# Kernel tuning notes

Measured on AMD Instinct MI355X. Metric: run time of the kernel, lower is better.

Reference implementation:

```python
import jax, jax.numpy as jnp
import numpy as np

PRE = 2000          # pre_wbf_detections
POST = 300          # post_wbf_detections
IOU_THRESH = 0.55   # wbf_iou_thresh
NUM_CLASSES = 5


def setup_inputs() -> dict:
    key = jax.random.key(0)
    k1, k2, k3, k4 = jax.random.split(key, 4)
    # realistic xyxy boxes in a 1024px image
    ctr = jax.random.uniform(k1, (PRE, 2), minval=0.0, maxval=1024.0)
    wh = jax.random.uniform(k2, (PRE, 2), minval=8.0, maxval=96.0)
    boxes = jnp.concatenate([ctr - wh / 2, ctr + wh / 2], axis=1)
    scores = jax.random.uniform(k3, (PRE, 1), minval=0.05, maxval=1.0)
    labels = jax.random.randint(k4, (PRE, 1), 0, NUM_CLASSES).astype(jnp.float32)
    x = jnp.concatenate([boxes, scores, labels], axis=1)  # (PRE, 6)
    return {"x": x}


def _iou_one_vs_many(box, mboxes):
    # torchvision-style box_iou of one box (4,) vs many (N,4)
    lt = jnp.maximum(box[:2], mboxes[:, :2])
    rb = jnp.minimum(box[2:], mboxes[:, 2:])
    wh = jnp.clip(rb - lt, 0.0)
    inter = wh[:, 0] * wh[:, 1]
    a1 = (box[2] - box[0]) * (box[3] - box[1])
    a2 = (mboxes[:, 2] - mboxes[:, 0]) * (mboxes[:, 3] - mboxes[:, 1])
    union = a1 + a2 - inter
    safe = jnp.where(union > 0, union, 1.0)
    return jnp.where(union > 0, inter / safe, 0.0)


def _wbf_forward(x):
    # Sequential WBF clustering. The torch code runs wbf() per unique class;
    # since a detection can only join a cluster of its own class and cluster
    # creation order within a class is preserved, a single sequential pass
    # with a class-equality check is mathematically identical (final result
    # is sorted by score, so per-class concatenation order is irrelevant).
    N = x.shape[0]
    # cluster state: score-weighted box sum, score sum, member count, class, valid
    init = (
        jnp.zeros((N, 4), x.dtype),   # sum of score*box per cluster
        jnp.zeros((N,), x.dtype),     # sum of scores per cluster
        jnp.zeros((N,), jnp.int32),   # member count per cluster
        jnp.zeros((N,), x.dtype),     # class id per cluster
        jnp.zeros((N,), bool),        # cluster slot valid
    )

    def step(carry, det):
        sum_wb, sum_s, cnt, cls, valid = carry
        box, score, c = det[:4], det[4], det[5]
        denom = jnp.where(valid, sum_s, 1.0)
        mboxes = sum_wb / denom[:, None]  # current merged boxes
        iou = _iou_one_vs_many(box, mboxes)
        match = valid & (cls == c) & (iou > IOU_THRESH)
        found = jnp.any(match)
        first = jnp.argmax(match)                  # first matching cluster
        n_valid = jnp.sum(valid).astype(jnp.int32)  # next free slot
        idx = jnp.where(found, first, n_valid)
        sum_wb = sum_wb.at[idx].add(score * box)
        sum_s = sum_s.at[idx].add(score)
        cnt = cnt.at[idx].add(1)
        cls = cls.at[idx].set(c)
        valid = valid.at[idx].set(True)
        return (sum_wb, sum_s, cnt, cls, valid), None

    (sum_wb, sum_s, cnt, cls, valid), _ = jax.lax.scan(step, init, x)

    denom = jnp.where(valid, sum_s, 1.0)
    boxes = sum_wb / denom[:, None]                              # weighted avg box
    scores = sum_s / jnp.maximum(cnt.astype(x.dtype), 1.0)       # mean score
    sort_key = jnp.where(valid, scores, -1.0)
    order = jnp.argsort(-sort_key)                               # descending by score
    top = order[:POST]
    vtop = valid[top]
    out = jnp.concatenate(
        [boxes[top], scores[top, None], cls[top, None]], axis=1)  # (POST, 6)
    return jnp.where(vtop[:, None], out, 0.0)


def reference(x):
    return _wbf_forward(x[:PRE])
```

## Files before the change

### kernel.cpp

```cpp
#include <hip/hip_runtime.h>

typedef unsigned long long u64;
typedef unsigned short u16;
typedef unsigned u32;
typedef unsigned char u8;

#define PRE   2000
#define POST  300
#define NCLS  5
#define CAP   512
#define INF   0x7fffffff
#define MAGIC 0x13579BDFu
#define NBLK  21
#define SORTB 20

#define MID 0x1.19999A8p-1

template <int K> struct IC { static constexpr int v = K; };
template <int N, typename F> __device__ __forceinline__ void unrollN(F&& f) {
    if constexpr (N > 0) { unrollN<N - 1>(f); f(IC<N - 1>{}); }
}

__device__ __forceinline__ u32 aload_acq(u32* p) {
    return __hip_atomic_load(p, __ATOMIC_ACQUIRE, __HIP_MEMORY_SCOPE_AGENT);
}

__device__ __forceinline__ float rlF(float v, int l) {
    return __uint_as_float((u32)__builtin_amdgcn_readlane((int)__float_as_uint(v), l));
}

__device__ __forceinline__ bool iou_pred(float bx0, float bx1, float bx2, float bx3,
                                         float a1, float m0, float m1, float m2, float m3,
                                         float a2) {
    const float ltx = fmaxf(bx0, m0), lty = fmaxf(bx1, m1);
    const float rbx = fminf(bx2, m2), rby = fminf(bx3, m3);
    const float wd = fmaxf(rbx - ltx, 0.f), hg = fmaxf(rby - lty, 0.f);
    const float inter = wd * hg;
    const float uni = (a1 + a2) - inter;
    return (uni > 0.f) && ((double)inter >= MID * (double)uni);
}

__global__ __launch_bounds__(512, 1) void wbf_all(const float* __restrict__ x,
                                                  u64* __restrict__ M,
                                                  u32* __restrict__ ctrl,
                                                  float* __restrict__ recs,
                                                  int* __restrict__ cnts,
                                                  float* __restrict__ out) {
#pragma clang fp contract(off)
    __shared__ __align__(16) char s_buf[58448];
    u8*  s_mtx = (u8*)s_buf;
    float (*s_det)[8]  = (float (*)[8])(s_buf + 32768);
    float (*s_dov)[16] = (float (*)[16])(s_buf + 49152);
    u16* s_list        = (u16*)(s_buf + 57344);
    u8*  s_ab          = (u8*)(s_buf + 58376);

    const int tid  = threadIdx.x;
    const int lane = tid & 63;
    const int wave = tid >> 6;
    const int b    = blockIdx.x;

    if (b == 0) {
        if (tid == 0) {
            for (int i = 0; i < NCLS; ++i)
                __hip_atomic_store(&ctrl[i], 0u, __ATOMIC_RELAXED, __HIP_MEMORY_SCOPE_AGENT);
            __hip_atomic_store(&ctrl[16], 0u, __ATOMIC_RELAXED, __HIP_MEMORY_SCOPE_AGENT);
            __hip_atomic_store(&ctrl[32], MAGIC, __ATOMIC_RELEASE, __HIP_MEMORY_SCOPE_AGENT);
        }
    } else {
        if (tid == 0) { while (aload_acq(&ctrl[32]) != MAGIC) {} }
    }
    __syncthreads();

    if (b == SORTB) {
        u64* keys = (u64*)s_buf;
        u32* hist = (u32*)(s_buf + 16384);
        u64* cand = (u64*)(s_buf + 32768);
        u32* part = (u32*)(s_buf + 36864);
        int* scal = (int*)(s_buf + 38912);

        for (int i = tid; i < 2048; i += 512) keys[i] = ~0ull;
        for (int h = tid; h < 4096; h += 512) hist[h] = 0u;
        if (tid == 0) scal[2] = 0;
        __syncthreads();
        if (tid == 0) { while (aload_acq(&ctrl[16]) < (u32)NCLS) {} }
        __syncthreads();

        int c[NCLS], off[NCLS];
        int n = 0;
        #pragma unroll
        for (int w = 0; w < NCLS; ++w) { c[w] = cnts[w]; off[w] = n; n += c[w]; }
        if (n > 2048) n = 2048;

        #pragma unroll
        for (int w = 0; w < NCLS; ++w) {
            const int cw = c[w], ow = off[w];
            for (int j = tid; j < cw; j += 512) {
                const float* r = recs + (size_t)(w * CAP + j) * 8;
                const unsigned sb = __float_as_uint(r[4]);
                const int g = ((const int*)r)[5];
                const int id = w * CAP + j;
                u64 key = ((u64)sb << 32) | ((u64)(unsigned)(0xFFFF - g) << 16) | (u64)id;
                keys[ow + j] = ~key;
            }
        }
        __syncthreads();

        for (int i = tid; i < n; i += 512)
            atomicAdd(&hist[(u32)(keys[i] >> 52)], 1u);
        __syncthreads();

        const int target = (POST < n) ? POST : n;
        u32 p = 0;
        #pragma unroll
        for (int k = 0; k < 8; ++k) p += hist[tid * 8 + k];
        part[tid] = p;
        __syncthreads();
        for (int o2 = 1; o2 < 512; o2 <<= 1) {
            const u32 v = part[tid];
            const u32 add = (tid >= o2) ? part[tid - o2] : 0u;
            __syncthreads();
            part[tid] = v + add;
            __syncthreads();
        }
        const u32 I = part[tid];
        const u32 E = I - p;
        if ((int)E < target && (int)I >= target) { scal[0] = tid; scal[1] = (int)E; }
        __syncthreads();
        const int T = scal[0];
        int cum = scal[1];
        int B = T * 8 + 7;
        for (int bb = T * 8; bb < T * 8 + 8; ++bb) {
            const int h = (int)hist[bb];
            if (cum + h >= target) { B = bb; break; }
            cum += h;
        }
        const int candCount = cum + (int)hist[B];

        if (candCount <= 512) {
            for (int i = tid; i < n; i += 512) {
                const u64 kk = keys[i];
                if ((int)(u32)(kk >> 52) <= B) {
                    const int pos = atomicAdd(&scal[2], 1);
                    cand[pos] = kk;
                }
            }
            __syncthreads();
            if (tid >= candCount) cand[tid] = ~0ull;
            __syncthreads();
            for (int kk2 = 2; kk2 <= 512; kk2 <<= 1) {
                for (int jj = kk2 >> 1; jj > 0; jj >>= 1) {
                    const int i = tid, ixj = i ^ jj;
                    if (ixj > i) {
                        const u64 a = cand[i], bb2 = cand[ixj];
                        const bool up = ((i & kk2) == 0);
                        if ((a > bb2) == up) { cand[i] = bb2; cand[ixj] = a; }
                    }
                    __syncthreads();
                }
            }
            if (tid < POST) {
                float* o = out + tid * 6;
                if (tid < target) {
                    const u64 key = ~cand[tid];
                    const int id = (int)(key & 0xFFFFull);
                    const float* rec = recs + (size_t)id * 8;
                    o[0] = rec[0]; o[1] = rec[1]; o[2] = rec[2]; o[3] = rec[3];
                    o[4] = __uint_as_float((unsigned)(key >> 32));
                    o[5] = (float)(id >> 9);
                } else {
                    o[0] = 0.f; o[1] = 0.f; o[2] = 0.f; o[3] = 0.f; o[4] = 0.f; o[5] = 0.f;
                }
            }
        } else {
            for (int kk2 = 2; kk2 <= 2048; kk2 <<= 1) {
                for (int jj = kk2 >> 1; jj > 0; jj >>= 1) {
                    for (int i = tid; i < 2048; i += 512) {
                        const int ixj = i ^ jj;
                        if (ixj > i) {
                            const u64 a = keys[i], bb2 = keys[ixj];
                            const bool up = ((i & kk2) == 0);
                            if ((a > bb2) == up) { keys[i] = bb2; keys[ixj] = a; }
                        }
                        __syncthreads();
                    }
                }
            }
            if (tid < POST) {
                float* o = out + tid * 6;
                if (tid < target) {
                    const u64 key = ~keys[tid];
                    const int id = (int)(key & 0xFFFFull);
                    const float* rec = recs + (size_t)id * 8;
                    o[0] = rec[0]; o[1] = rec[1]; o[2] = rec[2]; o[3] = rec[3];
                    o[4] = __uint_as_float((unsigned)(key >> 32));
                    o[5] = (float)(id >> 9);
                } else {
                    o[0] = 0.f; o[1] = 0.f; o[2] = 0.f; o[3] = 0.f; o[4] = 0.f; o[5] = 0.f;
                }
            }
        }
        return;
    }

    const int cls = b >> 2;
    const float mycls = (float)cls;

    int myn;
    {
        int* s_wc = (int*)s_buf;
        u64 wm[4]; int wcnt = 0;
        const int tb = wave * 256;
        #pragma unroll
        for (int i = 0; i < 4; ++i) {
            const int t = tb + i * 64 + lane;
            const bool pp = (t < PRE) && (x[t * 6 + 5] == mycls);
            wm[i] = __ballot(pp);
            wcnt += (int)__popcll(wm[i]);
        }
        if (lane == 0) s_wc[wave] = wcnt;
        __syncthreads();
        int off = 0, tot = 0;
        #pragma unroll
        for (int w = 0; w < 8; ++w) {
            const int cw = s_wc[w];
            off += (w < wave) ? cw : 0;
            tot += cw;
        }
        #pragma unroll
        for (int i = 0; i < 4; ++i) {
            const int t = tb + i * 64 + lane;
            const bool pp = ((wm[i] >> lane) & 1ull) != 0ull;
            const int pos = off + (int)__popcll(wm[i] & (((u64)1 << lane) - 1ull));
            if (pp && pos < CAP) s_list[pos] = (u16)t;
            off += (int)__popcll(wm[i]);
        }
        myn = (tot > CAP) ? CAP : tot;
        __syncthreads();
    }

    {
        float qc0[8], qc1[8], qc2[8], qc3[8], ac[8];
        unrollN<8>([&](auto k_) {
            constexpr int K = decltype(k_)::v;
            const int c = K * 64 + lane;
            qc0[K] = 0.f; qc1[K] = 0.f; qc2[K] = 0.f; qc3[K] = 0.f; ac[K] = 0.f;
            if (c < myn) {
                const int g = s_list[c];
                const float* p = x + g * 6;
                const float b0 = p[0], b1 = p[1], b2 = p[2], b3 = p[3], sc = p[4];
                qc0[K] = (sc * b0) / sc; qc1[K] = (sc * b1) / sc;
                qc2[K] = (sc * b2) / sc; qc3[K] = (sc * b3) / sc;
                ac[K] = (qc2[K] - qc0[K]) * (qc3[K] - qc1[K]);
            }
        });
        const int slice = (b & 3) * 8 + wave;
        const int rlo = slice * 16;
        const int rhi = (rlo + 16 < myn) ? rlo + 16 : myn;
        for (int r = rlo; r < rhi; ++r) {
            const int g = s_list[r];
            const float* p = x + g * 6;
            const float bx0 = p[0], bx1 = p[1], bx2 = p[2], bx3 = p[3];
            const float a1 = (bx2 - bx0) * (bx3 - bx1);
            const int Wmax = r >> 6;
            unrollN<8>([&](auto w_) {
                constexpr int W = decltype(w_)::v;
                if (W <= Wmax) {
                    const int c = W * 64 + lane;
                    const bool pred = (c < r) &&
                        iou_pred(bx0, bx1, bx2, bx3, a1, qc0[W], qc1[W], qc2[W], qc3[W], ac[W]);
                    const u64 bits = __ballot(pred);
                    if (lane == 0) M[((size_t)(cls * CAP + r)) * 8 + W] = bits;
                }
            });
        }
    }
    __threadfence();
    if (lane == 0)
        __hip_atomic_fetch_add(&ctrl[cls], 1u, __ATOMIC_RELEASE, __HIP_MEMORY_SCOPE_AGENT);

    if ((b & 3) != 0) return;

    if (lane == 0) { while (aload_acq(&ctrl[cls]) < 32u) {} }
    __syncthreads();
    {
        const ulonglong2* Mg = (const ulonglong2*)(M + (size_t)cls * CAP * 8);
        ulonglong2* Ml = (ulonglong2*)s_mtx;
        const int nit = myn * 4;
        for (int it = tid; it < nit; it += 512) Ml[it] = Mg[it];
    }
    for (int rr = tid; rr < myn; rr += 512) {
        const int g = s_list[rr];
        const float* p = x + g * 6;
        const float b0 = p[0], b1 = p[1], b2 = p[2], b3 = p[3], sc = p[4];
        s_det[rr][0] = b0; s_det[rr][1] = b1; s_det[rr][2] = b2; s_det[rr][3] = b3;
        s_det[rr][4] = sc; s_det[rr][5] = (b2 - b0) * (b3 - b1);
        ((int*)s_det[rr])[6] = g;
    }
    if (tid < 64) s_ab[tid] = 0;
    __syncthreads();
    if (wave != 0) return;

    u32 aliveB = 0;
    int dirtyCnt = 0;
    bool consA = false;
    int resCode = 0, resIdx = 0;
    float dR0 = 0.f, dR1 = 0.f, dR2 = 0.f, dR3 = 0.f, dRa = 0.f;
    float dS0 = 0.f, dS1 = 0.f, dS2 = 0.f, dS3 = 0.f, dSs = 0.f;
    int dRank = INF, dGi = 0, dCnt = 0;
    float rm0 = 0.f, rm1 = 0.f, rm2 = 0.f, rm3 = 0.f, rma = 0.f;

    auto resolve = [&](int r, float bx0, float bx1, float bx2, float bx3,
                       float sc, float a1, u32 rowByte) {
        const u32 mC = rowByte & aliveB;
        const u64 balC = __ballot(mC != 0u);
        int rank_c = INF;
        if (balC) {
            const int wl = (int)__builtin_ctzll(balC);
            const u32 byte = (u32)__builtin_amdgcn_readlane((int)mC, wl);
            rank_c = wl * 8 + (int)__builtin_ctz(byte);
        }
        const int rcs = (rank_c == INF) ? 0 : rank_c;
        const float cb0 = s_det[rcs][0], cb1 = s_det[rcs][1];
        const float cb2 = s_det[rcs][2], cb3 = s_det[rcs][3];
        const float csc = s_det[rcs][4];
        const int cgi = ((const int*)s_det[rcs])[6];

        int rank_d = INF, di = -1;
        if (dirtyCnt > 0) {
            const int DN = (dirtyCnt < 64) ? dirtyCnt : 64;
            const bool p = (lane < DN) &&
                iou_pred(bx0, bx1, bx2, bx3, a1, dR0, dR1, dR2, dR3, dRa);
            const int myrk = p ? dRank : INF;
            u64 mk = __ballot(p);
            while (mk) {
                const int l = (int)__builtin_ctzll(mk);
                mk &= mk - 1;
                const int rk = __builtin_amdgcn_readlane(myrk, l);
                if (rk < rank_d) { rank_d = rk; di = l; }
            }
            for (int dd = 64; dd < dirtyCnt; ++dd) {
                const float* dv = s_dov[dd];
                if (iou_pred(bx0, bx1, bx2, bx3, a1, dv[0], dv[1], dv[2], dv[3], dv[4])) {
                    const int rk = ((const int*)dv)[10];
                    if (rk < rank_d) { rank_d = rk; di = dd; }
                }
            }
        }
        if (rank_c == INF && rank_d == INF) {
            aliveB |= ((r >> 3) == lane) ? (1u << (r & 7)) : 0u;
            resCode = 0;
        } else if (rank_c < rank_d) {
            const int rc = rank_c;
            aliveB &= ~(((rc >> 3) == lane) ? (1u << (rc & 7)) : 0u);
            const float ns0 = (csc * cb0) + sc * bx0;
            const float ns1 = (csc * cb1) + sc * bx1;
            const float ns2 = (csc * cb2) + sc * bx2;
            const float ns3 = (csc * cb3) + sc * bx3;
            const float nss = csc + sc;
            const float nm0 = ns0 / nss, nm1 = ns1 / nss;
            const float nm2 = ns2 / nss, nm3 = ns3 / nss;
            const float nar = (nm2 - nm0) * (nm3 - nm1);
            const int D = dirtyCnt;
            if (D < 64) {
                if (lane == D) {
                    dR0 = nm0; dR1 = nm1; dR2 = nm2; dR3 = nm3; dRa = nar;
                    dS0 = ns0; dS1 = ns1; dS2 = ns2; dS3 = ns3; dSs = nss;
                    dRank = rc; dGi = cgi; dCnt = 2;
                }
            } else if (D < 128) {
                if (lane == 0) {
                    float* dv = s_dov[D];
                    dv[0] = nm0; dv[1] = nm1; dv[2] = nm2; dv[3] = nm3; dv[4] = nar;
                    dv[5] = ns0; dv[6] = ns1; dv[7] = ns2; dv[8] = ns3; dv[9] = nss;
                    ((int*)dv)[10] = rc; ((int*)dv)[11] = cgi; ((int*)dv)[12] = 2;
                }
            }
            dirtyCnt++;
            resCode = 1; resIdx = D;
            rm0 = nm0; rm1 = nm1; rm2 = nm2; rm3 = nm3; rma = nar;
        } else {
            float f0, f1, f2, f3, fs; int nct;
            if (di < 64) {
                f0 = rlF(dS0, di) + sc * bx0; f1 = rlF(dS1, di) + sc * bx1;
                f2 = rlF(dS2, di) + sc * bx2; f3 = rlF(dS3, di) + sc * bx3;
                fs = rlF(dSs, di) + sc;
                nct = __builtin_amdgcn_readlane(dCnt, di) + 1;
            } else {
                const float* dv = s_dov[di];
                f0 = dv[5] + sc * bx0; f1 = dv[6] + sc * bx1;
                f2 = dv[7] + sc * bx2; f3 = dv[8] + sc * bx3;
                fs = dv[9] + sc;
                nct = ((const int*)dv)[12] + 1;
            }
            const float nm0 = f0 / fs, nm1 = f1 / fs, nm2 = f2 / fs, nm3 = f3 / fs;
            const float nar = (nm2 - nm0) * (nm3 - nm1);
            if (di < 64) {
                if (lane == di) {
                    dR0 = nm0; dR1 = nm1; dR2 = nm2; dR3 = nm3; dRa = nar;
                    dS0 = f0; dS1 = f1; dS2 = f2; dS3 = f3; dSs = fs; dCnt = nct;
                }
            } else {
                if (lane == 0) {
                    float* dw = s_dov[di];
                    dw[0] = nm0; dw[1] = nm1; dw[2] = nm2; dw[3] = nm3; dw[4] = nar;
                    dw[5] = f0; dw[6] = f1; dw[7] = f2; dw[8] = f3; dw[9] = fs;
                    ((int*)dw)[12] = nct;
                }
            }
            rm0 = nm0; rm1 = nm1; rm2 = nm2; rm3 = nm3; rma = nar;
            resCode = 2; resIdx = di;
        }
    };

    unrollN<8>([&](auto k_) {
        constexpr int K = decltype(k_)::v;
        const int r0 = K * 64;
        if (r0 < myn) {
            const int cnt = (myn - r0 < 64) ? (myn - r0) : 64;
            const bool valid = lane < cnt;
            const u64 validM = (cnt == 64) ? ~0ull : (((u64)1 << cnt) - 1ull);
            u64 orv = 0ull;
            {
                const int rr = r0 + (valid ? lane : 0);
                const u64* rp = (const u64*)&s_mtx[(size_t)rr * 64];
                const u64* av = (const u64*)s_ab;
                unrollN<8>([&](auto w_) {
                    constexpr int W = decltype(w_)::v;
                    if (W < K)       orv |= rp[W] & av[W];
                    else if (W == K) orv |= rp[W];
                });
            }
            const u64 rowW = __ballot(valid && orv != 0ull);
            float4 db = make_float4(0.f, 0.f, 0.f, 0.f);
            float2 de = make_float2(1.f, 0.f);
            if (valid) {
                db = *(const float4*)&s_det[r0 + lane][0];
                de = *(const float2*)&s_det[r0 + lane][4];
            }
            u64 dmask = 0ull;
            if (!consA) {
                const int DN = (dirtyCnt < 64) ? dirtyCnt : 64;
                for (int d = 0; d < DN; ++d) {
                    const float m0 = rlF(dR0, d), m1 = rlF(dR1, d);
                    const float m2 = rlF(dR2, d), m3 = rlF(dR3, d);
                    const float ma = rlF(dRa, d);
                    const bool pp = valid && iou_pred(db.x, db.y, db.z, db.w, de.y,
                                                     m0, m1, m2, m3, ma);
                    if (pp) dmask |= 1ull << d;
                }
            }
            u64 danyb = __ballot(dmask != 0ull);

            u32 prB[8]; int prP[8];
            {
                u64 t = consA ? validM : ((danyb | rowW) & validM);
                #pragma unroll
                for (int i = 0; i < 8; ++i) {
                    const int f = t ? (int)__builtin_ctzll(t) : 0;
                    prP[i] = t ? f : 64;
                    prB[i] = (u32)s_mtx[(size_t)(r0 + f) * 64 + lane];
                    t &= t - 1ull;
                }
            }

            int p = 0;
            while (p < cnt) {
                u64 vm = consA ? validM : ((danyb | rowW) & validM);
                vm &= ~(((u64)1 << p) - 1ull);
                const int F = vm ? (int)__builtin_ctzll(vm) : cnt;
                {
                    const int lo = r0 + p, h2 = r0 + F;
                    int s = lo - 8 * lane; s = (s > 0) ? s : 0;
                    int e = h2 - 8 * lane; e = (e < 8) ? e : 8;
                    if (e > s) aliveB |= ((0xFFu >> (8 - (e - s))) << s);
                }
                s_ab[lane] = (u8)aliveB;
                if (F >= cnt) break;
                const int r = r0 + F;
                u32 rowByte = 0u; bool hit = false;
                #pragma unroll
                for (int i = 0; i < 8; ++i)
                    if (prP[i] == F) { rowByte = prB[i]; hit = true; }
                if (!hit) rowByte = (u32)s_mtx[(size_t)r * 64 + lane];
                const u64 balCq = __ballot((rowByte & aliveB) != 0u);
                const bool Fdirty = consA || (((danyb >> F) & 1ull) != 0ull);
                if (!Fdirty && balCq == 0ull) {
                    aliveB |= ((r >> 3) == lane) ? (1u << (r & 7)) : 0u;
                    s_ab[lane] = (u8)aliveB;
                } else {
                    const float bx0 = rlF(db.x, F), bx1 = rlF(db.y, F);
                    const float bx2 = rlF(db.z, F), bx3 = rlF(db.w, F);
                    const float sc = rlF(de.x, F), a1 = rlF(de.y, F);
                    resolve(r, bx0, bx1, bx2, bx3, sc, a1, rowByte);
                    s_ab[lane] = (u8)aliveB;
                    if (resCode != 0) {
                        const int idx = resIdx;
                        if (idx < 64) {
                            const bool pnew = valid && (lane > F) &&
                                iou_pred(db.x, db.y, db.z, db.w, de.y,
                                         rm0, rm1, rm2, rm3, rma);
                            const u64 nb = __ballot(pnew);
                            dmask = (dmask & ~(1ull << idx)) | (((nb >> lane) & 1ull) << idx);
                            danyb = __ballot(dmask != 0ull);
                        } else {
                            consA = true;
                        }
                    }
                }
                p = F + 1;
            }
        }
    });

    int wo = 0;
    for (int Kw = 0; Kw < 8; ++Kw) {
        u64 am = 0ull;
        #pragma unroll
        for (int bb = 0; bb < 8; ++bb)
            am |= (u64)(u32)(u8)__builtin_amdgcn_readlane((int)aliveB, Kw * 8 + bb) << (8 * bb);
        const int j = Kw * 64 + lane;
        const bool pred = (am >> lane) & 1ull;
        if (pred) {
            const int pos = wo + (int)__popcll(am & (((u64)1 << lane) - 1));
            const float b0 = s_det[j][0], b1 = s_det[j][1];
            const float b2 = s_det[j][2], b3 = s_det[j][3];
            const float sc = s_det[j][4];
            const int g = ((const int*)s_det[j])[6];
            float* rec = recs + (size_t)(cls * CAP + pos) * 8;
            rec[0] = (sc * b0) / sc; rec[1] = (sc * b1) / sc;
            rec[2] = (sc * b2) / sc; rec[3] = (sc * b3) / sc;
            rec[4] = sc;
            ((int*)rec)[5] = g;
        }
        wo += (int)__popcll(am);
    }
    const int demit = (dirtyCnt < 128) ? dirtyCnt : 128;
    {
        const int dreg = (demit < 64) ? demit : 64;
        if (lane < dreg) {
            float* rec = recs + (size_t)(cls * CAP + wo + lane) * 8;
            rec[0] = dR0; rec[1] = dR1; rec[2] = dR2; rec[3] = dR3;
            rec[4] = dSs / (float)dCnt;
            ((int*)rec)[5] = dGi;
        }
        for (int d = 64 + lane; d < demit; d += 64) {
            const float* dv = s_dov[d];
            float* rec = recs + (size_t)(cls * CAP + wo + d) * 8;
            rec[0] = dv[0]; rec[1] = dv[1]; rec[2] = dv[2]; rec[3] = dv[3];
            rec[4] = dv[9] / (float)(((const int*)dv)[12]);
            ((int*)rec)[5] = ((const int*)dv)[11];
        }
    }
    if (lane == 0) cnts[cls] = wo + demit;
    __threadfence();
    if (lane == 0)
        __hip_atomic_fetch_add(&ctrl[16], 1u, __ATOMIC_RELEASE, __HIP_MEMORY_SCOPE_AGENT);
}

extern "C" void kernel_launch(void* const* d_in, const int* in_sizes, int n_in,
                              void* d_out, int out_size, void* d_ws, size_t ws_size,
                              hipStream_t stream) {
    const float* x = (const float*)d_in[0];
    float* out = (float*)d_out;
    u64* M      = (u64*)d_ws;
    u32* ctrl   = (u32*)((char*)d_ws + (size_t)NCLS * CAP * 8 * 8);
    int* cnts   = (int*)((char*)d_ws + (size_t)NCLS * CAP * 8 * 8 + 256);
    float* recs = (float*)((char*)d_ws + (size_t)NCLS * CAP * 8 * 8 + 512);
    wbf_all<<<NBLK, 512, 0, stream>>>(x, M, ctrl, recs, cnts, out);
}
```

Baseline: 110.1 us.

## Stream per-class results into sorter, widen dirty mask, prefetch rows via readlane

The sort block no longer waits for all classes to finish. It polls per-class ready flags and ingests each class's records and histogram counts as soon as that class completes, so sorting work overlaps with the tail of the other classes. The IoU matrix builder loads each wave's 16 row boxes once into lanes and broadcasts them with readlane instead of doing a global load per row. The sequential resolve now tracks dirty clusters up to 128 in a two-word mask, which avoids falling back to the conservative path, and it skips the union and divide math when no lane has a positive intersection. Records are appended in completion order, so tie-breaking must still hold through the key encoding.

New measurement: 106.6 us. 3.2% less time.

```diff
diff --git a/kernel.cpp b/kernel.cpp
--- a/kernel.cpp
+++ b/kernel.cpp
@@ -63,7 +63,8 @@
         if (tid == 0) {
             for (int i = 0; i < NCLS; ++i)
                 __hip_atomic_store(&ctrl[i], 0u, __ATOMIC_RELAXED, __HIP_MEMORY_SCOPE_AGENT);
-            __hip_atomic_store(&ctrl[16], 0u, __ATOMIC_RELAXED, __HIP_MEMORY_SCOPE_AGENT);
+            for (int i = 0; i < NCLS; ++i)
+                __hip_atomic_store(&ctrl[20 + i], 0u, __ATOMIC_RELAXED, __HIP_MEMORY_SCOPE_AGENT);
             __hip_atomic_store(&ctrl[32], MAGIC, __ATOMIC_RELEASE, __HIP_MEMORY_SCOPE_AGENT);
         }
     } else {
@@ -80,34 +81,40 @@
 
         for (int i = tid; i < 2048; i += 512) keys[i] = ~0ull;
         for (int h = tid; h < 4096; h += 512) hist[h] = 0u;
-        if (tid == 0) scal[2] = 0;
+        if (tid == 0) { scal[2] = 0; scal[3] = 0; }
         __syncthreads();
-        if (tid == 0) { while (aload_acq(&ctrl[16]) < (u32)NCLS) {} }
-        __syncthreads();
-
-        int c[NCLS], off[NCLS];
-        int n = 0;
-        #pragma unroll
-        for (int w = 0; w < NCLS; ++w) { c[w] = cnts[w]; off[w] = n; n += c[w]; }
-        if (n > 2048) n = 2048;
-
-        #pragma unroll
-        for (int w = 0; w < NCLS; ++w) {
-            const int cw = c[w], ow = off[w];
-            for (int j = tid; j < cw; j += 512) {
-                const float* r = recs + (size_t)(w * CAP + j) * 8;
+
+        u32 done = 0;
+        while (done != 0x1Fu) {
+            if (tid == 0) {
+                int pick = -1;
+                while (pick < 0) {
+                    #pragma unroll
+                    for (int c = 0; c < NCLS; ++c)
+                        if (!((done >> c) & 1u) && aload_acq(&ctrl[20 + c]) == 1u) { pick = c; break; }
+                }
+                scal[4] = pick;
+                scal[5] = scal[3];
+            }
+            __syncthreads();
+            const int c = scal[4];
+            const int base = scal[5];
+            const int cw = cnts[c];
+            int take = cw; if (base + take > 2048) take = 2048 - base;
+            for (int j = tid; j < take; j += 512) {
+                const float* r = recs + (size_t)(c * CAP + j) * 8;
                 const unsigned sb = __float_as_uint(r[4]);
                 const int g = ((const int*)r)[5];
-                const int id = w * CAP + j;
+                const int id = c * CAP + j;
                 u64 key = ((u64)sb << 32) | ((u64)(unsigned)(0xFFFF - g) << 16) | (u64)id;
-                keys[ow + j] = ~key;
-            }
-        }
-        __syncthreads();
-
-        for (int i = tid; i < n; i += 512)
-            atomicAdd(&hist[(u32)(keys[i] >> 52)], 1u);
-        __syncthreads();
+                keys[base + j] = ~key;
+                atomicAdd(&hist[(u32)((~key) >> 52)], 1u);
+            }
+            if (tid == 0) scal[3] = base + take;
+            done |= 1u << c;
+            __syncthreads();
+        }
+        const int n = scal[3];
 
         const int target = (POST < n) ? POST : n;
         u32 p = 0;
@@ -256,22 +263,31 @@
         const int slice = (b & 3) * 8 + wave;
         const int rlo = slice * 16;
         const int rhi = (rlo + 16 < myn) ? rlo + 16 : myn;
-        for (int r = rlo; r < rhi; ++r) {
-            const int g = s_list[r];
-            const float* p = x + g * 6;
-            const float bx0 = p[0], bx1 = p[1], bx2 = p[2], bx3 = p[3];
-            const float a1 = (bx2 - bx0) * (bx3 - bx1);
-            const int Wmax = r >> 6;
-            unrollN<8>([&](auto w_) {
-                constexpr int W = decltype(w_)::v;
-                if (W <= Wmax) {
-                    const int c = W * 64 + lane;
-                    const bool pred = (c < r) &&
-                        iou_pred(bx0, bx1, bx2, bx3, a1, qc0[W], qc1[W], qc2[W], qc3[W], ac[W]);
-                    const u64 bits = __ballot(pred);
-                    if (lane == 0) M[((size_t)(cls * CAP + r)) * 8 + W] = bits;
-                }
-            });
+        const int nr = rhi - rlo;
+        if (nr > 0) {
+            float rv0 = 0.f, rv1 = 0.f, rv2 = 0.f, rv3 = 0.f;
+            if (lane < nr) {
+                const int g = s_list[rlo + lane];
+                const float* p = x + g * 6;
+                rv0 = p[0]; rv1 = p[1]; rv2 = p[2]; rv3 = p[3];
+            }
+            for (int i = 0; i < nr; ++i) {
+                const int r = rlo + i;
+                const float bx0 = rlF(rv0, i), bx1 = rlF(rv1, i);
+                const float bx2 = rlF(rv2, i), bx3 = rlF(rv3, i);
+                const float a1 = (bx2 - bx0) * (bx3 - bx1);
+                const int Wmax = r >> 6;
+                unrollN<8>([&](auto w_) {
+                    constexpr int W = decltype(w_)::v;
+                    if (W <= Wmax) {
+                        const int c = W * 64 + lane;
+                        const bool pred = (c < r) &&
+                            iou_pred(bx0, bx1, bx2, bx3, a1, qc0[W], qc1[W], qc2[W], qc3[W], ac[W]);
+                        const u64 bits = __ballot(pred);
+                        if (lane == 0) M[((size_t)(cls * CAP + r)) * 8 + W] = bits;
+                    }
+                });
+            }
         }
     }
     __threadfence();
@@ -338,7 +354,8 @@
                 const int rk = __builtin_amdgcn_readlane(myrk, l);
                 if (rk < rank_d) { rank_d = rk; di = l; }
             }
-            for (int dd = 64; dd < dirtyCnt; ++dd) {
+            const int DH2 = (dirtyCnt < 128) ? dirtyCnt : 128;
+            for (int dd = 64; dd < DH2; ++dd) {
                 const float* dv = s_dov[dd];
                 if (iou_pred(bx0, bx1, bx2, bx3, a1, dv[0], dv[1], dv[2], dv[3], dv[4])) {
                     const int rk = ((const int*)dv)[10];
@@ -437,19 +454,42 @@
                 db = *(const float4*)&s_det[r0 + lane][0];
                 de = *(const float2*)&s_det[r0 + lane][4];
             }
-            u64 dmask = 0ull;
+            u64 dmaskLo = 0ull, dmaskHi = 0ull;
             if (!consA) {
                 const int DN = (dirtyCnt < 64) ? dirtyCnt : 64;
                 for (int d = 0; d < DN; ++d) {
                     const float m0 = rlF(dR0, d), m1 = rlF(dR1, d);
                     const float m2 = rlF(dR2, d), m3 = rlF(dR3, d);
-                    const float ma = rlF(dRa, d);
-                    const bool pp = valid && iou_pred(db.x, db.y, db.z, db.w, de.y,
-                                                     m0, m1, m2, m3, ma);
-                    if (pp) dmask |= 1ull << d;
-                }
-            }
-            u64 danyb = __ballot(dmask != 0ull);
+                    const float ltx = fmaxf(db.x, m0), lty = fmaxf(db.y, m1);
+                    const float rbx = fminf(db.z, m2), rby = fminf(db.w, m3);
+                    const float wd = fmaxf(rbx - ltx, 0.f), hg = fmaxf(rby - lty, 0.f);
+                    const float inter = wd * hg;
+                    if (__ballot(valid && inter > 0.f)) {
+                        const float ma = rlF(dRa, d);
+                        const float uni = (de.y + ma) - inter;
+                        const bool pp = valid && (uni > 0.f) &&
+                                        ((double)inter >= MID * (double)uni);
+                        if (pp) dmaskLo |= 1ull << d;
+                    }
+                }
+                const int DH = (dirtyCnt < 128) ? dirtyCnt : 128;
+                for (int dd = 64; dd < DH; ++dd) {
+                    const float* dv = s_dov[dd];
+                    const float m0 = dv[0], m1 = dv[1], m2 = dv[2], m3 = dv[3];
+                    const float ltx = fmaxf(db.x, m0), lty = fmaxf(db.y, m1);
+                    const float rbx = fminf(db.z, m2), rby = fminf(db.w, m3);
+                    const float wd = fmaxf(rbx - ltx, 0.f), hg = fmaxf(rby - lty, 0.f);
+                    const float inter = wd * hg;
+                    if (__ballot(valid && inter > 0.f)) {
+                        const float ma = dv[4];
+                        const float uni = (de.y + ma) - inter;
+                        const bool pp = valid && (uni > 0.f) &&
+                                        ((double)inter >= MID * (double)uni);
+                        if (pp) dmaskHi |= 1ull << (dd - 64);
+                    }
+                }
+            }
+            u64 danyb = __ballot((dmaskLo | dmaskHi) != 0ull);
 
             u32 prB[8]; int prP[8];
             {
@@ -495,13 +535,17 @@
                     s_ab[lane] = (u8)aliveB;
                     if (resCode != 0) {
                         const int idx = resIdx;
-                        if (idx < 64) {
+                        if (idx < 128) {
                             const bool pnew = valid && (lane > F) &&
                                 iou_pred(db.x, db.y, db.z, db.w, de.y,
                                          rm0, rm1, rm2, rm3, rma);
                             const u64 nb = __ballot(pnew);
-                            dmask = (dmask & ~(1ull << idx)) | (((nb >> lane) & 1ull) << idx);
-                            danyb = __ballot(dmask != 0ull);
+                            const u64 bit = (nb >> lane) & 1ull;
+                            if (idx < 64)
+                                dmaskLo = (dmaskLo & ~(1ull << idx)) | (bit << idx);
+                            else
+                                dmaskHi = (dmaskHi & ~(1ull << (idx - 64))) | (bit << (idx - 64));
+                            danyb = __ballot((dmaskLo | dmaskHi) != 0ull);
                         } else {
                             consA = true;
                         }
@@ -554,7 +598,7 @@
     if (lane == 0) cnts[cls] = wo + demit;
     __threadfence();
     if (lane == 0)
-        __hip_atomic_fetch_add(&ctrl[16], 1u, __ATOMIC_RELEASE, __HIP_MEMORY_SCOPE_AGENT);
+        __hip_atomic_store(&ctrl[20 + cls], 1u, __ATOMIC_RELEASE, __HIP_MEMORY_SCOPE_AGENT);
 }
 
 extern "C" void kernel_launch(void* const* d_in, const int* in_sizes, int n_in,
```

## Split fused persistent kernel into matrix, scan and sort launches

Applied to the files above, without the earlier changes.

Replaces the single 21-block kernel, which used global atomic flags and spin-waits to order its stages, with three kernel launches (IoU matrix, per-class sequential scan, top-K sort) that rely on stream ordering. The matrix stage now preloads row boxes into lanes and broadcasts them with readlane, and it writes per-class detection records that the scan stage copies into LDS as float4 vectors. The scan stage's dirty-cluster tracking grows from 64 to 128 entries by splitting the mask into low and high halves. This removes spin-wait and fence overhead but adds two extra launch latencies and a global round trip for the detection records.

New measurement: 104.9 us. 1.05x faster.

```diff
diff --git a/kernel.cpp b/kernel.cpp
--- a/kernel.cpp
+++ b/kernel.cpp
@@ -10,19 +10,12 @@
 #define NCLS  5
 #define CAP   512
 #define INF   0x7fffffff
-#define MAGIC 0x13579BDFu
-#define NBLK  21
-#define SORTB 20
 
 #define MID 0x1.19999A8p-1
 
 template <int K> struct IC { static constexpr int v = K; };
 template <int N, typename F> __device__ __forceinline__ void unrollN(F&& f) {
     if constexpr (N > 0) { unrollN<N - 1>(f); f(IC<N - 1>{}); }
-}
-
-__device__ __forceinline__ u32 aload_acq(u32* p) {
-    return __hip_atomic_load(p, __ATOMIC_ACQUIRE, __HIP_MEMORY_SCOPE_AGENT);
 }
 
 __device__ __forceinline__ float rlF(float v, int l) {
@@ -40,203 +33,49 @@
     return (uni > 0.f) && ((double)inter >= MID * (double)uni);
 }
 
-__global__ __launch_bounds__(512, 1) void wbf_all(const float* __restrict__ x,
-                                                  u64* __restrict__ M,
-                                                  u32* __restrict__ ctrl,
-                                                  float* __restrict__ recs,
-                                                  int* __restrict__ cnts,
-                                                  float* __restrict__ out) {
+__global__ __launch_bounds__(512, 1) void wbf_matrix(const float* __restrict__ x,
+                                                     u64* __restrict__ M,
+                                                     float* __restrict__ dets,
+                                                     int* __restrict__ nlist) {
 #pragma clang fp contract(off)
-    __shared__ __align__(16) char s_buf[58448];
-    u8*  s_mtx = (u8*)s_buf;
-    float (*s_det)[8]  = (float (*)[8])(s_buf + 32768);
-    float (*s_dov)[16] = (float (*)[16])(s_buf + 49152);
-    u16* s_list        = (u16*)(s_buf + 57344);
-    u8*  s_ab          = (u8*)(s_buf + 58376);
+    __shared__ int s_wc[8];
+    __shared__ u16 s_list[CAP];
 
     const int tid  = threadIdx.x;
     const int lane = tid & 63;
     const int wave = tid >> 6;
     const int b    = blockIdx.x;
-
-    if (b == 0) {
-        if (tid == 0) {
-            for (int i = 0; i < NCLS; ++i)
-                __hip_atomic_store(&ctrl[i], 0u, __ATOMIC_RELAXED, __HIP_MEMORY_SCOPE_AGENT);
-            __hip_atomic_store(&ctrl[16], 0u, __ATOMIC_RELAXED, __HIP_MEMORY_SCOPE_AGENT);
-            __hip_atomic_store(&ctrl[32], MAGIC, __ATOMIC_RELEASE, __HIP_MEMORY_SCOPE_AGENT);
-        }
-    } else {
-        if (tid == 0) { while (aload_acq(&ctrl[32]) != MAGIC) {} }
-    }
-    __syncthreads();
-
-    if (b == SORTB) {
-        u64* keys = (u64*)s_buf;
-        u32* hist = (u32*)(s_buf + 16384);
-        u64* cand = (u64*)(s_buf + 32768);
-        u32* part = (u32*)(s_buf + 36864);
-        int* scal = (int*)(s_buf + 38912);
-
-        for (int i = tid; i < 2048; i += 512) keys[i] = ~0ull;
-        for (int h = tid; h < 4096; h += 512) hist[h] = 0u;
-        if (tid == 0) scal[2] = 0;
-        __syncthreads();
-        if (tid == 0) { while (aload_acq(&ctrl[16]) < (u32)NCLS) {} }
-        __syncthreads();
-
-        int c[NCLS], off[NCLS];
-        int n = 0;
-        #pragma unroll
-        for (int w = 0; w < NCLS; ++w) { c[w] = cnts[w]; off[w] = n; n += c[w]; }
-        if (n > 2048) n = 2048;
-
-        #pragma unroll
-        for (int w = 0; w < NCLS; ++w) {
-            const int cw = c[w], ow = off[w];
-            for (int j = tid; j < cw; j += 512) {
-                const float* r = recs + (size_t)(w * CAP + j) * 8;
-                const unsigned sb = __float_as_uint(r[4]);
-                const int g = ((const int*)r)[5];
-                const int id = w * CAP + j;
-                u64 key = ((u64)sb << 32) | ((u64)(unsigned)(0xFFFF - g) << 16) | (u64)id;
-                keys[ow + j] = ~key;
-            }
-        }
-        __syncthreads();
-
-        for (int i = tid; i < n; i += 512)
-            atomicAdd(&hist[(u32)(keys[i] >> 52)], 1u);
-        __syncthreads();
-
-        const int target = (POST < n) ? POST : n;
-        u32 p = 0;
-        #pragma unroll
-        for (int k = 0; k < 8; ++k) p += hist[tid * 8 + k];
-        part[tid] = p;
-        __syncthreads();
-        for (int o2 = 1; o2 < 512; o2 <<= 1) {
-            const u32 v = part[tid];
-            const u32 add = (tid >= o2) ? part[tid - o2] : 0u;
-            __syncthreads();
-            part[tid] = v + add;
-            __syncthreads();
-        }
-        const u32 I = part[tid];
-        const u32 E = I - p;
-        if ((int)E < target && (int)I >= target) { scal[0] = tid; scal[1] = (int)E; }
-        __syncthreads();
-        const int T = scal[0];
-        int cum = scal[1];
-        int B = T * 8 + 7;
-        for (int bb = T * 8; bb < T * 8 + 8; ++bb) {
-            const int h = (int)hist[bb];
-            if (cum + h >= target) { B = bb; break; }
-            cum += h;
-        }
-        const int candCount = cum + (int)hist[B];
-
-        if (candCount <= 512) {
-            for (int i = tid; i < n; i += 512) {
-                const u64 kk = keys[i];
-                if ((int)(u32)(kk >> 52) <= B) {
-                    const int pos = atomicAdd(&scal[2], 1);
-                    cand[pos] = kk;
-                }
-            }
-            __syncthreads();
-            if (tid >= candCount) cand[tid] = ~0ull;
-            __syncthreads();
-            for (int kk2 = 2; kk2 <= 512; kk2 <<= 1) {
-                for (int jj = kk2 >> 1; jj > 0; jj >>= 1) {
-                    const int i = tid, ixj = i ^ jj;
-                    if (ixj > i) {
-                        const u64 a = cand[i], bb2 = cand[ixj];
-                        const bool up = ((i & kk2) == 0);
-                        if ((a > bb2) == up) { cand[i] = bb2; cand[ixj] = a; }
-                    }
-                    __syncthreads();
-                }
-            }
-            if (tid < POST) {
-                float* o = out + tid * 6;
-                if (tid < target) {
-                    const u64 key = ~cand[tid];
-                    const int id = (int)(key & 0xFFFFull);
-                    const float* rec = recs + (size_t)id * 8;
-                    o[0] = rec[0]; o[1] = rec[1]; o[2] = rec[2]; o[3] = rec[3];
-                    o[4] = __uint_as_float((unsigned)(key >> 32));
-                    o[5] = (float)(id >> 9);
-                } else {
-                    o[0] = 0.f; o[1] = 0.f; o[2] = 0.f; o[3] = 0.f; o[4] = 0.f; o[5] = 0.f;
-                }
-            }
-        } else {
-            for (int kk2 = 2; kk2 <= 2048; kk2 <<= 1) {
-                for (int jj = kk2 >> 1; jj > 0; jj >>= 1) {
-                    for (int i = tid; i < 2048; i += 512) {
-                        const int ixj = i ^ jj;
-                        if (ixj > i) {
-                            const u64 a = keys[i], bb2 = keys[ixj];
-                            const bool up = ((i & kk2) == 0);
-                            if ((a > bb2) == up) { keys[i] = bb2; keys[ixj] = a; }
-                        }
-                        __syncthreads();
-                    }
-                }
-            }
-            if (tid < POST) {
-                float* o = out + tid * 6;
-                if (tid < target) {
-                    const u64 key = ~keys[tid];
-                    const int id = (int)(key & 0xFFFFull);
-                    const float* rec = recs + (size_t)id * 8;
-                    o[0] = rec[0]; o[1] = rec[1]; o[2] = rec[2]; o[3] = rec[3];
-                    o[4] = __uint_as_float((unsigned)(key >> 32));
-                    o[5] = (float)(id >> 9);
-                } else {
-                    o[0] = 0.f; o[1] = 0.f; o[2] = 0.f; o[3] = 0.f; o[4] = 0.f; o[5] = 0.f;
-                }
-            }
-        }
-        return;
-    }
-
-    const int cls = b >> 2;
+    const int cls  = b >> 2;
     const float mycls = (float)cls;
 
-    int myn;
-    {
-        int* s_wc = (int*)s_buf;
-        u64 wm[4]; int wcnt = 0;
-        const int tb = wave * 256;
-        #pragma unroll
-        for (int i = 0; i < 4; ++i) {
-            const int t = tb + i * 64 + lane;
-            const bool pp = (t < PRE) && (x[t * 6 + 5] == mycls);
-            wm[i] = __ballot(pp);
-            wcnt += (int)__popcll(wm[i]);
-        }
-        if (lane == 0) s_wc[wave] = wcnt;
-        __syncthreads();
-        int off = 0, tot = 0;
-        #pragma unroll
-        for (int w = 0; w < 8; ++w) {
-            const int cw = s_wc[w];
-            off += (w < wave) ? cw : 0;
-            tot += cw;
-        }
-        #pragma unroll
-        for (int i = 0; i < 4; ++i) {
-            const int t = tb + i * 64 + lane;
-            const bool pp = ((wm[i] >> lane) & 1ull) != 0ull;
-            const int pos = off + (int)__popcll(wm[i] & (((u64)1 << lane) - 1ull));
-            if (pp && pos < CAP) s_list[pos] = (u16)t;
-            off += (int)__popcll(wm[i]);
-        }
-        myn = (tot > CAP) ? CAP : tot;
-        __syncthreads();
-    }
+    u64 wm[4]; int wcnt = 0;
+    const int tb = wave * 256;
+    #pragma unroll
+    for (int i = 0; i < 4; ++i) {
+        const int t = tb + i * 64 + lane;
+        const bool pp = (t < PRE) && (x[t * 6 + 5] == mycls);
+        wm[i] = __ballot(pp);
+        wcnt += (int)__popcll(wm[i]);
+    }
+    if (lane == 0) s_wc[wave] = wcnt;
+    __syncthreads();
+    int off = 0, tot = 0;
+    #pragma unroll
+    for (int w = 0; w < 8; ++w) {
+        const int cw = s_wc[w];
+        off += (w < wave) ? cw : 0;
+        tot += cw;
+    }
+    #pragma unroll
+    for (int i = 0; i < 4; ++i) {
+        const int t = tb + i * 64 + lane;
+        const bool pp = ((wm[i] >> lane) & 1ull) != 0ull;
+        const int pos = off + (int)__popcll(wm[i] & (((u64)1 << lane) - 1ull));
+        if (pp && pos < CAP) s_list[pos] = (u16)t;
+        off += (int)__popcll(wm[i]);
+    }
+    const int myn = (tot > CAP) ? CAP : tot;
+    __syncthreads();
 
     {
         float qc0[8], qc1[8], qc2[8], qc3[8], ac[8];
@@ -256,45 +95,78 @@
         const int slice = (b & 3) * 8 + wave;
         const int rlo = slice * 16;
         const int rhi = (rlo + 16 < myn) ? rlo + 16 : myn;
-        for (int r = rlo; r < rhi; ++r) {
-            const int g = s_list[r];
+        const int nr = rhi - rlo;
+        if (nr > 0) {
+            float rv0 = 0.f, rv1 = 0.f, rv2 = 0.f, rv3 = 0.f;
+            if (lane < nr) {
+                const int g = s_list[rlo + lane];
+                const float* p = x + g * 6;
+                rv0 = p[0]; rv1 = p[1]; rv2 = p[2]; rv3 = p[3];
+            }
+            for (int i = 0; i < nr; ++i) {
+                const int r = rlo + i;
+                const float bx0 = rlF(rv0, i), bx1 = rlF(rv1, i);
+                const float bx2 = rlF(rv2, i), bx3 = rlF(rv3, i);
+                const float a1 = (bx2 - bx0) * (bx3 - bx1);
+                const int Wmax = r >> 6;
+                unrollN<8>([&](auto w_) {
+                    constexpr int W = decltype(w_)::v;
+                    if (W <= Wmax) {
+                        const int c = W * 64 + lane;
+                        const bool pred = (c < r) &&
+                            iou_pred(bx0, bx1, bx2, bx3, a1, qc0[W], qc1[W], qc2[W], qc3[W], ac[W]);
+                        const u64 bits = __ballot(pred);
+                        if (lane == 0) M[((size_t)(cls * CAP + r)) * 8 + W] = bits;
+                    }
+                });
+            }
+        }
+    }
+
+    if ((b & 3) == 0) {
+        for (int rr = tid; rr < myn; rr += 512) {
+            const int g = s_list[rr];
             const float* p = x + g * 6;
-            const float bx0 = p[0], bx1 = p[1], bx2 = p[2], bx3 = p[3];
-            const float a1 = (bx2 - bx0) * (bx3 - bx1);
-            const int Wmax = r >> 6;
-            unrollN<8>([&](auto w_) {
-                constexpr int W = decltype(w_)::v;
-                if (W <= Wmax) {
-                    const int c = W * 64 + lane;
-                    const bool pred = (c < r) &&
-                        iou_pred(bx0, bx1, bx2, bx3, a1, qc0[W], qc1[W], qc2[W], qc3[W], ac[W]);
-                    const u64 bits = __ballot(pred);
-                    if (lane == 0) M[((size_t)(cls * CAP + r)) * 8 + W] = bits;
-                }
-            });
-        }
-    }
-    __threadfence();
-    if (lane == 0)
-        __hip_atomic_fetch_add(&ctrl[cls], 1u, __ATOMIC_RELEASE, __HIP_MEMORY_SCOPE_AGENT);
-
-    if ((b & 3) != 0) return;
-
-    if (lane == 0) { while (aload_acq(&ctrl[cls]) < 32u) {} }
-    __syncthreads();
+            const float b0 = p[0], b1 = p[1], b2 = p[2], b3 = p[3], sc = p[4];
+            float* dr = dets + (size_t)(cls * CAP + rr) * 8;
+            dr[0] = b0; dr[1] = b1; dr[2] = b2; dr[3] = b3;
+            dr[4] = sc; dr[5] = (b2 - b0) * (b3 - b1);
+            ((int*)dr)[6] = g; ((int*)dr)[7] = 0;
+        }
+        if (tid == 0) nlist[cls] = myn;
+    }
+}
+
+__global__ __launch_bounds__(512, 1) void wbf_scan(const u64* __restrict__ M,
+                                                   const float* __restrict__ dets,
+                                                   const int* __restrict__ nlist,
+                                                   float* __restrict__ recs,
+                                                   int* __restrict__ cnts) {
+#pragma clang fp contract(off)
+    __shared__ __align__(16) char s_buf[57408];
+    u8*  s_mtx = (u8*)s_buf;
+    float (*s_det)[8]  = (float (*)[8])(s_buf + 32768);
+    float (*s_dov)[16] = (float (*)[16])(s_buf + 49152);
+    u8*  s_ab          = (u8*)(s_buf + 57344);
+
+    const int tid  = threadIdx.x;
+    const int lane = tid & 63;
+    const int wave = tid >> 6;
+    const int cls  = blockIdx.x;
+
+    const int myn = nlist[cls];
+
     {
         const ulonglong2* Mg = (const ulonglong2*)(M + (size_t)cls * CAP * 8);
         ulonglong2* Ml = (ulonglong2*)s_mtx;
         const int nit = myn * 4;
         for (int it = tid; it < nit; it += 512) Ml[it] = Mg[it];
     }
-    for (int rr = tid; rr < myn; rr += 512) {
-        const int g = s_list[rr];
-        const float* p = x + g * 6;
-        const float b0 = p[0], b1 = p[1], b2 = p[2], b3 = p[3], sc = p[4];
-        s_det[rr][0] = b0; s_det[rr][1] = b1; s_det[rr][2] = b2; s_det[rr][3] = b3;
-        s_det[rr][4] = sc; s_det[rr][5] = (b2 - b0) * (b3 - b1);
-        ((int*)s_det[rr])[6] = g;
+    {
+        const float4* Dg = (const float4*)(dets + (size_t)cls * CAP * 8);
+        float4* Dl = (float4*)s_det;
+        const int nit = myn * 2;
+        for (int it = tid; it < nit; it += 512) Dl[it] = Dg[it];
     }
     if (tid < 64) s_ab[tid] = 0;
     __syncthreads();
@@ -338,7 +210,8 @@
                 const int rk = __builtin_amdgcn_readlane(myrk, l);
                 if (rk < rank_d) { rank_d = rk; di = l; }
             }
-            for (int dd = 64; dd < dirtyCnt; ++dd) {
+            const int DH2 = (dirtyCnt < 128) ? dirtyCnt : 128;
+            for (int dd = 64; dd < DH2; ++dd) {
                 const float* dv = s_dov[dd];
                 if (iou_pred(bx0, bx1, bx2, bx3, a1, dv[0], dv[1], dv[2], dv[3], dv[4])) {
                     const int rk = ((const int*)dv)[10];
@@ -437,7 +310,7 @@
                 db = *(const float4*)&s_det[r0 + lane][0];
                 de = *(const float2*)&s_det[r0 + lane][4];
             }
-            u64 dmask = 0ull;
+            u64 dmaskLo = 0ull, dmaskHi = 0ull;
             if (!consA) {
                 const int DN = (dirtyCnt < 64) ? dirtyCnt : 64;
                 for (int d = 0; d < DN; ++d) {
@@ -446,10 +319,17 @@
                     const float ma = rlF(dRa, d);
                     const bool pp = valid && iou_pred(db.x, db.y, db.z, db.w, de.y,
                                                      m0, m1, m2, m3, ma);
-                    if (pp) dmask |= 1ull << d;
-                }
-            }
-            u64 danyb = __ballot(dmask != 0ull);
+                    if (pp) dmaskLo |= 1ull << d;
+                }
+                const int DH = (dirtyCnt < 128) ? dirtyCnt : 128;
+                for (int dd = 64; dd < DH; ++dd) {
+                    const float* dv = s_dov[dd];
+                    const bool pp = valid && iou_pred(db.x, db.y, db.z, db.w, de.y,
+                                                     dv[0], dv[1], dv[2], dv[3], dv[4]);
+                    if (pp) dmaskHi |= 1ull << (dd - 64);
+                }
+            }
+            u64 danyb = __ballot((dmaskLo | dmaskHi) != 0ull);
 
             u32 prB[8]; int prP[8];
             {
@@ -495,13 +375,17 @@
                     s_ab[lane] = (u8)aliveB;
                     if (resCode != 0) {
                         const int idx = resIdx;
-                        if (idx < 64) {
+                        if (idx < 128) {
                             const bool pnew = valid && (lane > F) &&
                                 iou_pred(db.x, db.y, db.z, db.w, de.y,
                                          rm0, rm1, rm2, rm3, rma);
                             const u64 nb = __ballot(pnew);
-                            dmask = (dmask & ~(1ull << idx)) | (((nb >> lane) & 1ull) << idx);
-                            danyb = __ballot(dmask != 0ull);
+                            const u64 bit = (nb >> lane) & 1ull;
+                            if (idx < 64)
+                                dmaskLo = (dmaskLo & ~(1ull << idx)) | (bit << idx);
+                            else
+                                dmaskHi = (dmaskHi & ~(1ull << (idx - 64))) | (bit << (idx - 64));
+                            danyb = __ballot((dmaskLo | dmaskHi) != 0ull);
                         } else {
                             consA = true;
                         }
@@ -552,9 +436,136 @@
         }
     }
     if (lane == 0) cnts[cls] = wo + demit;
-    __threadfence();
-    if (lane == 0)
-        __hip_atomic_fetch_add(&ctrl[16], 1u, __ATOMIC_RELEASE, __HIP_MEMORY_SCOPE_AGENT);
+}
+
+__global__ __launch_bounds__(512, 1) void wbf_sort(const float* __restrict__ recs,
+                                                   const int* __restrict__ cnts,
+                                                   float* __restrict__ out) {
+    __shared__ __align__(16) char s_buf[39168];
+    u64* keys = (u64*)s_buf;
+    u32* hist = (u32*)(s_buf + 16384);
+    u64* cand = (u64*)(s_buf + 32768);
+    u32* part = (u32*)(s_buf + 36864);
+    int* scal = (int*)(s_buf + 38912);
+
+    const int tid = threadIdx.x;
+
+    for (int i = tid; i < 2048; i += 512) keys[i] = ~0ull;
+    for (int h = tid; h < 4096; h += 512) hist[h] = 0u;
+    if (tid == 0) scal[2] = 0;
+    __syncthreads();
+
+    int c[NCLS], off[NCLS];
+    int n = 0;
+    #pragma unroll
+    for (int w = 0; w < NCLS; ++w) { c[w] = cnts[w]; off[w] = n; n += c[w]; }
+    if (n > 2048) n = 2048;
+
+    #pragma unroll
+    for (int w = 0; w < NCLS; ++w) {
+        const int cw = c[w], ow = off[w];
+        for (int j = tid; j < cw && ow + j < 2048; j += 512) {
+            const float* r = recs + (size_t)(w * CAP + j) * 8;
+            const unsigned sb = __float_as_uint(r[4]);
+            const int g = ((const int*)r)[5];
+            const int id = w * CAP + j;
+            u64 key = ((u64)sb << 32) | ((u64)(unsigned)(0xFFFF - g) << 16) | (u64)id;
+            keys[ow + j] = ~key;
+            atomicAdd(&hist[(u32)((~key) >> 52)], 1u);
+        }
+    }
+    __syncthreads();
+
+    const int target = (POST < n) ? POST : n;
+    u32 p = 0;
+    #pragma unroll
+    for (int k = 0; k < 8; ++k) p += hist[tid * 8 + k];
+    part[tid] = p;
+    __syncthreads();
+    for (int o2 = 1; o2 < 512; o2 <<= 1) {
+        const u32 v = part[tid];
+        const u32 add = (tid >= o2) ? part[tid - o2] : 0u;
+        __syncthreads();
+        part[tid] = v + add;
+        __syncthreads();
+    }
+    const u32 I = part[tid];
+    const u32 E = I - p;
+    if ((int)E < target && (int)I >= target) { scal[0] = tid; scal[1] = (int)E; }
+    __syncthreads();
+    const int T = scal[0];
+    int cum = scal[1];
+    int B = T * 8 + 7;
+    for (int bb = T * 8; bb < T * 8 + 8; ++bb) {
+        const int h = (int)hist[bb];
+        if (cum + h >= target) { B = bb; break; }
+        cum += h;
+    }
+    const int candCount = cum + (int)hist[B];
+
+    if (candCount <= 512) {
+        for (int i = tid; i < n; i += 512) {
+            const u64 kk = keys[i];
+            if ((int)(u32)(kk >> 52) <= B) {
+                const int pos = atomicAdd(&scal[2], 1);
+                cand[pos] = kk;
+            }
+        }
+        __syncthreads();
+        if (tid >= candCount) cand[tid] = ~0ull;
+        __syncthreads();
+        for (int kk2 = 2; kk2 <= 512; kk2 <<= 1) {
+            for (int jj = kk2 >> 1; jj > 0; jj >>= 1) {
+                const int i = tid, ixj = i ^ jj;
+                if (ixj > i) {
+                    const u64 a = cand[i], bb2 = cand[ixj];
+                    const bool up = ((i & kk2) == 0);
+                    if ((a > bb2) == up) { cand[i] = bb2; cand[ixj] = a; }
+                }
+                __syncthreads();
+            }
+        }
+        if (tid < POST) {
+            float* o = out + tid * 6;
+            if (tid < target) {
+                const u64 key = ~cand[tid];
+                const int id = (int)(key & 0xFFFFull);
+                const float* rec = recs + (size_t)id * 8;
+                o[0] = rec[0]; o[1] = rec[1]; o[2] = rec[2]; o[3] = rec[3];
+                o[4] = __uint_as_float((unsigned)(key >> 32));
+                o[5] = (float)(id >> 9);
+            } else {
+                o[0] = 0.f; o[1] = 0.f; o[2] = 0.f; o[3] = 0.f; o[4] = 0.f; o[5] = 0.f;
+            }
+        }
+    } else {
+        for (int kk2 = 2; kk2 <= 2048; kk2 <<= 1) {
+            for (int jj = kk2 >> 1; jj > 0; jj >>= 1) {
+                for (int i = tid; i < 2048; i += 512) {
+                    const int ixj = i ^ jj;
+                    if (ixj > i) {
+                        const u64 a = keys[i], bb2 = keys[ixj];
+                        const bool up = ((i & kk2) == 0);
+                        if ((a > bb2) == up) { keys[i] = bb2; keys[ixj] = a; }
+                    }
+                }
+                __syncthreads();
+            }
+        }
+        if (tid < POST) {
+            float* o = out + tid * 6;
+            if (tid < target) {
+                const u64 key = ~keys[tid];
+                const int id = (int)(key & 0xFFFFull);
+                const float* rec = recs + (size_t)id * 8;
+                o[0] = rec[0]; o[1] = rec[1]; o[2] = rec[2]; o[3] = rec[3];
+                o[4] = __uint_as_float((unsigned)(key >> 32));
+                o[5] = (float)(id >> 9);
+            } else {
+                o[0] = 0.f; o[1] = 0.f; o[2] = 0.f; o[3] = 0.f; o[4] = 0.f; o[5] = 0.f;
+            }
+        }
+    }
 }
 
 extern "C" void kernel_launch(void* const* d_in, const int* in_sizes, int n_in,
@@ -562,9 +573,12 @@
                               hipStream_t stream) {
     const float* x = (const float*)d_in[0];
     float* out = (float*)d_out;
-    u64* M      = (u64*)d_ws;
-    u32* ctrl   = (u32*)((char*)d_ws + (size_t)NCLS * CAP * 8 * 8);
-    int* cnts   = (int*)((char*)d_ws + (size_t)NCLS * CAP * 8 * 8 + 256);
-    float* recs = (float*)((char*)d_ws + (size_t)NCLS * CAP * 8 * 8 + 512);
-    wbf_all<<<NBLK, 512, 0, stream>>>(x, M, ctrl, recs, cnts, out);
-}
+    u64*   M     = (u64*)d_ws;
+    float* dets  = (float*)((char*)d_ws + 163840);
+    float* recs  = (float*)((char*)d_ws + 163840 + 81920);
+    int*   cnts  = (int*)((char*)d_ws + 163840 + 163840);
+    int*   nlist = cnts + 16;
+    wbf_matrix<<<NCLS * 4, 512, 0, stream>>>(x, M, dets, nlist);
+    wbf_scan<<<NCLS, 512, 0, stream>>>(M, dets, nlist, recs, cnts);
+    wbf_sort<<<1, 512, 0, stream>>>(recs, cnts, out);
+}
```
